# Performance work log

Hardware: AMD Instinct MI355X
Metric: run time of the kernel (lower is better)

The kernel has to match this reference:

```python
import jax, jax.numpy as jnp
import numpy as np

C_IN, C_OUT, KH, KW = 64, 128, 3, 3
STRIDE, PAD, DIL = 1, 1, 1
EPS = 1e-5


def setup_inputs() -> dict:
    key = jax.random.key(0)
    ks = jax.random.split(key, 7)
    B, H, W = 8, 112, 112
    x = jax.random.normal(ks[0], (B, C_IN, H, W), dtype=jnp.float32)
    # offset conv: produces 2*KH*KW offset channels; small init keeps offsets sane
    w_off = jax.random.normal(ks[1], (2 * KH * KW, C_IN, KH, KW), dtype=jnp.float32) * 0.01
    b_off = jax.random.normal(ks[2], (2 * KH * KW,), dtype=jnp.float32) * 0.01
    # deformable conv weight/bias
    fan_in = C_IN * KH * KW
    w_dcn = jax.random.normal(ks[3], (C_OUT, C_IN, KH, KW), dtype=jnp.float32) / np.sqrt(fan_in)
    b_dcn = jax.random.normal(ks[4], (C_OUT,), dtype=jnp.float32) * 0.01
    gamma = jnp.ones((C_OUT,), dtype=jnp.float32)
    beta = jnp.zeros((C_OUT,), dtype=jnp.float32)
    return {"x": x, "w_off": w_off, "b_off": b_off, "w_dcn": w_dcn,
            "b_dcn": b_dcn, "gamma": gamma, "beta": beta}


def _conv2d(x, w, b):
    y = jax.lax.conv_general_dilated(
        x, w, window_strides=(STRIDE, STRIDE),
        padding=((PAD, PAD), (PAD, PAD)),
        rhs_dilation=(DIL, DIL),
        dimension_numbers=("NCHW", "OIHW", "NCHW"))
    return y + b[None, :, None, None]


def _deform_conv(x, offset, w, b):
    # x: [B,C,H,W]; offset: [B, 2*KH*KW, Ho, Wo] with (dy, dx) pairs per tap
    B, C, H, W = x.shape
    KK = KH * KW
    Ho, Wo = offset.shape[2], offset.shape[3]
    off = offset.reshape(B, KK, 2, Ho, Wo)
    ky = (jnp.arange(KK) // KW).astype(jnp.float32)  # kernel row per tap
    kx = (jnp.arange(KK) % KW).astype(jnp.float32)
    base_y = (jnp.arange(Ho) * STRIDE - PAD).astype(jnp.float32)
    base_x = (jnp.arange(Wo) * STRIDE - PAD).astype(jnp.float32)
    # sampling positions [B, KK, Ho, Wo]
    py = off[:, :, 0] + base_y[None, None, :, None] + (ky * DIL)[None, :, None, None]
    px = off[:, :, 1] + base_x[None, None, None, :] + (kx * DIL)[None, :, None, None]

    y0 = jnp.floor(py)
    x0 = jnp.floor(px)
    wy1 = py - y0  # weight for y0+1
    wx1 = px - x0
    y0i = y0.astype(jnp.int32)
    x0i = x0.astype(jnp.int32)

    x_flat = x.reshape(B, C, H * W)

    def gather_corner(yi, xi, wgt):
        # yi, xi, wgt: [B, KK, Ho, Wo]
        valid = (yi >= 0) & (yi < H) & (xi >= 0) & (xi < W)
        idx = jnp.clip(yi, 0, H - 1) * W + jnp.clip(xi, 0, W - 1)
        idx = idx.reshape(B, -1)  # [B, KK*Ho*Wo]
        vals = jnp.take_along_axis(x_flat, idx[:, None, :], axis=2)  # [B, C, N]
        coef = (wgt * valid.astype(wgt.dtype)).reshape(B, 1, -1)
        return vals * coef

    samp = (gather_corner(y0i,     x0i,     (1 - wy1) * (1 - wx1))
            + gather_corner(y0i,     x0i + 1, (1 - wy1) * wx1)
            + gather_corner(y0i + 1, x0i,     wy1 * (1 - wx1))
            + gather_corner(y0i + 1, x0i + 1, wy1 * wx1))
    samp = samp.reshape(B, C, KK, Ho, Wo)
    out = jnp.einsum("bckhw,ock->bohw", samp, w.reshape(w.shape[0], C, KK))
    return out + b[None, :, None, None]


def reference(x, w_off, b_off, w_dcn, b_dcn, gamma, beta):
    offset = _conv2d(x, w_off, b_off)
    y = _deform_conv(x, offset, w_dcn, b_dcn)
    # BatchNorm2d (training mode: biased batch stats) + ReLU
    mean = jnp.mean(y, axis=(0, 2, 3))
    var = jnp.var(y, axis=(0, 2, 3))
    yhat = (y - mean[None, :, None, None]) * jax.lax.rsqrt(var + EPS)[None, :, None, None]
    y = gamma[None, :, None, None] * yhat + beta[None, :, None, None]
    return jax.nn.relu(y)
```

## Files before the change

kernel.cpp:

```cpp
#include <hip/hip_runtime.h>

#define H    112
#define W    112
#define HW   12544
#define CIN  64
#define COUT 128
#define BATCH 8
#define KK   9
#define OFFC 18
#define EPS  1e-5f
#define TP   32
#define KDIM 576
#define KHALF 288
#define KPAD2 296
#define NB   3136

typedef unsigned short ushort;
typedef unsigned int uint;
typedef __attribute__((ext_vector_type(8))) short short8;
typedef __attribute__((ext_vector_type(8))) ushort ushort8;
typedef __attribute__((ext_vector_type(4))) float floatx4;

__device__ __forceinline__ ushort f2bf(float f) {
  uint u = __float_as_uint(f);
  u = (u + 0x7FFFu + ((u >> 16) & 1u)) >> 16;
  return (ushort)u;
}

__device__ __forceinline__ uint pack_bf2(float f0, float f1) {
  uint u0 = __float_as_uint(f0) + 0x8000u;
  uint u1 = __float_as_uint(f1) + 0x8000u;
  return __builtin_amdgcn_perm(u1, u0, 0x07060302u);
}

__device__ __forceinline__ float bf2f(ushort u) {
  return __uint_as_float(((uint)u) << 16);
}

__global__ __launch_bounds__(256) void k_transpose_x(
    const float* __restrict__ x, ushort* __restrict__ xTb) {
  __shared__ float tile[64][65];
  int b = blockIdx.y;
  int p0 = blockIdx.x * 64;
  int tid = threadIdx.x;
  int j = tid & 63, cb = tid >> 6;
#pragma unroll
  for (int i = 0; i < 16; ++i) {
    int ci = cb * 16 + i;
    tile[ci][j] = x[((size_t)(b * CIN + ci)) * HW + p0 + j];
  }
  __syncthreads();
  int px = tid >> 2, ciq = tid & 3;
#pragma unroll
  for (int g = 0; g < 4; ++g) {
    int ci = ciq * 16 + g * 4;
    uint lo = pack_bf2(tile[ci + 0][px], tile[ci + 1][px]);
    uint hi = pack_bf2(tile[ci + 2][px], tile[ci + 3][px]);
    *(uint2*)&xTb[((size_t)b * HW + p0 + px) * 64 + ci] = make_uint2(lo, hi);
  }
}

__global__ __launch_bounds__(256) void k_prep_w(
    const float* __restrict__ w_off, const float* __restrict__ w_dcn,
    ushort* __restrict__ w_offT, ushort* __restrict__ w_mf) {
  int i = blockIdx.x * 256 + threadIdx.x;
  if (i < 32 * KDIM) {
    int oc = i / KDIM, k = i - oc * KDIM;
    int kk = k >> 6, ci = k & 63;
    float v = (oc < OFFC) ? w_off[(oc * CIN + ci) * KK + kk] : 0.f;
    w_offT[i] = f2bf(v);
  } else if (i < 32 * KDIM + COUT * KDIM) {
    int jj = i - 32 * KDIM;
    int co = jj / KDIM, k = jj - co * KDIM;
    int h = k / KHALF, r = k - h * KHALF;
    int kk = r >> 5, cil = r & 31;
    int ci = h * 32 + cil;
    w_mf[jj] = f2bf(w_dcn[(co * CIN + ci) * KK + kk]);
  }
}

__global__ __launch_bounds__(256) void k_offset_conv(
    const ushort* __restrict__ xTb, const ushort* __restrict__ w_offT,
    const float* __restrict__ bias, float* __restrict__ out) {
  int b = blockIdx.y;
  int wave = threadIdx.x >> 6, lane = threadIdx.x & 63;
  int row16 = lane & 15, quad = lane >> 4;
  int p = blockIdx.x * 64 + wave * 16 + row16;
  int ho = p / W, wo = p - ho * W;
  const ushort* xb = xTb + (size_t)b * HW * 64;

  short8 Bf[18];
#pragma unroll
  for (int ks = 0; ks < 18; ++ks) {
    int kk = ks >> 1;
    int ci0 = (ks & 1) * 32 + quad * 8;
    int kh = kk / 3, kw = kk - kh * 3;
    int yy = ho + kh - 1, xx = wo + kw - 1;
    bool valid = (yy >= 0) & (yy < H) & (xx >= 0) & (xx < W);
    short8 v = {0, 0, 0, 0, 0, 0, 0, 0};
    if (valid) v = *(const short8*)(xb + ((size_t)(yy * W + xx) << 6) + ci0);
    Bf[ks] = v;
  }
  floatx4 acc0 = {0.f, 0.f, 0.f, 0.f}, acc1 = acc0;
  const ushort* wa0 = w_offT + row16 * KDIM + quad * 8;
  const ushort* wa1 = w_offT + (16 + row16) * KDIM + quad * 8;
#pragma unroll
  for (int ks = 0; ks < 18; ++ks) {
    short8 A0 = *(const short8*)(wa0 + ks * 32);
    short8 A1 = *(const short8*)(wa1 + ks * 32);
    acc0 = __builtin_amdgcn_mfma_f32_16x16x32_bf16(A0, Bf[ks], acc0, 0, 0, 0);
    acc1 = __builtin_amdgcn_mfma_f32_16x16x32_bf16(A1, Bf[ks], acc1, 0, 0, 0);
  }
  float* ob = out + (size_t)b * OFFC * HW;
#pragma unroll
  for (int reg = 0; reg < 4; ++reg) {
    int oc = quad * 4 + reg;
    ob[(size_t)oc * HW + p] = acc0[reg] + bias[oc];
    int oc1 = 16 + oc;
    if (oc1 < OFFC) ob[(size_t)oc1 * HW + p] = acc1[reg] + bias[oc1];
  }
}

__global__ __launch_bounds__(256) void k_deform(
    const ushort* __restrict__ xTb, const float* __restrict__ off,
    const ushort* __restrict__ w_mf, ushort* __restrict__ y,
    float* __restrict__ psT) {
  __shared__ float4 s_w[KK][TP];
  __shared__ int4   s_i[KK][TP];
  __shared__ ushort samp[TP][KPAD2];

  int b = blockIdx.y;
  int p0 = blockIdx.x * TP;
  int bid = blockIdx.y * gridDim.x + blockIdx.x;
  int tid = threadIdx.x;
  const ushort* xb = xTb + (size_t)b * HW * 64;

  for (int it = tid; it < KK * TP; it += 256) {
    int kk = it >> 5;
    int px = it & 31;
    int p = p0 + px;
    int ho = p / W, wo = p - ho * W;
    float dy = off[((size_t)b * OFFC + 2 * kk) * HW + p];
    float dx = off[((size_t)b * OFFC + 2 * kk + 1) * HW + p];
    float py = dy + (float)(ho - 1 + kk / 3);
    float pxx = dx + (float)(wo - 1 + kk % 3);
    float y0f = floorf(py), x0f = floorf(pxx);
    float wy1 = py - y0f, wx1 = pxx - x0f;
    int y0 = (int)y0f, x0 = (int)x0f;
    int y1 = y0 + 1, x1 = x0 + 1;
    float vy0 = (y0 >= 0 && y0 < H) ? 1.f : 0.f;
    float vy1 = (y1 >= 0 && y1 < H) ? 1.f : 0.f;
    float vx0 = (x0 >= 0 && x0 < W) ? 1.f : 0.f;
    float vx1 = (x1 >= 0 && x1 < W) ? 1.f : 0.f;
    int cy0 = min(max(y0, 0), H - 1), cy1 = min(max(y1, 0), H - 1);
    int cx0 = min(max(x0, 0), W - 1), cx1 = min(max(x1, 0), W - 1);
    s_w[kk][px] = make_float4((1.f - wy1) * (1.f - wx1) * vy0 * vx0,
                              (1.f - wy1) * wx1 * vy0 * vx1,
                              wy1 * (1.f - wx1) * vy1 * vx0,
                              wy1 * wx1 * vy1 * vx1);
    s_i[kk][px] = make_int4((cy0 * W + cx0) << 6, (cy0 * W + cx1) << 6,
                            (cy1 * W + cx0) << 6, (cy1 * W + cx1) << 6);
  }
  __syncthreads();

  int wave = tid >> 6, lane = tid & 63;
  int row16 = lane & 15, quad = lane >> 4;
  int koff = quad * 8;
  int co_base = wave * 32;
  const ushort* wa0 = w_mf + (size_t)(co_base + row16) * KDIM + koff;
  const ushort* wa1 = w_mf + (size_t)(co_base + 16 + row16) * KDIM + koff;

  floatx4 acc00 = {0.f, 0.f, 0.f, 0.f}, acc01 = acc00, acc10 = acc00, acc11 = acc00;

  for (int h = 0; h < 2; ++h) {
#pragma unroll
    for (int r = 0; r < 5; ++r) {
      int it = tid + r * 256;
      if (it < 1152) {
        int px = it / 36;
        int rem = it - px * 36;
        int kk = rem >> 2;
        int cig = rem & 3;
        int cil0 = cig * 8;
        int cio = h * 32 + cil0;
        float4 wv = s_w[kk][px];
        int4 iv = s_i[kk][px];
        ushort8 c0 = *(const ushort8*)(xb + iv.x + cio);
        ushort8 c1 = *(const ushort8*)(xb + iv.y + cio);
        ushort8 c2 = *(const ushort8*)(xb + iv.z + cio);
        ushort8 c3 = *(const ushort8*)(xb + iv.w + cio);
        uint pk[4];
#pragma unroll
        for (int g = 0; g < 4; ++g) {
          float r0 = wv.x * bf2f(c0[2 * g])     + wv.y * bf2f(c1[2 * g]) +
                     wv.z * bf2f(c2[2 * g])     + wv.w * bf2f(c3[2 * g]);
          float r1 = wv.x * bf2f(c0[2 * g + 1]) + wv.y * bf2f(c1[2 * g + 1]) +
                     wv.z * bf2f(c2[2 * g + 1]) + wv.w * bf2f(c3[2 * g + 1]);
          pk[g] = pack_bf2(r0, r1);
        }
        *(uint4*)&samp[px][kk * 32 + cil0] = make_uint4(pk[0], pk[1], pk[2], pk[3]);
      }
    }
    __syncthreads();

    const ushort* sb0 = &samp[row16][koff];
    const ushort* sb1 = &samp[16 + row16][koff];
    const ushort* a0 = wa0 + h * KHALF;
    const ushort* a1 = wa1 + h * KHALF;
#pragma unroll
    for (int ks = 0; ks < 9; ++ks) {
      short8 A0 = *(const short8*)(a0 + ks * 32);
      short8 A1 = *(const short8*)(a1 + ks * 32);
      short8 B0 = *(const short8*)(sb0 + ks * 32);
      short8 B1 = *(const short8*)(sb1 + ks * 32);
      acc00 = __builtin_amdgcn_mfma_f32_16x16x32_bf16(A0, B0, acc00, 0, 0, 0);
      acc01 = __builtin_amdgcn_mfma_f32_16x16x32_bf16(A0, B1, acc01, 0, 0, 0);
      acc10 = __builtin_amdgcn_mfma_f32_16x16x32_bf16(A1, B0, acc10, 0, 0, 0);
      acc11 = __builtin_amdgcn_mfma_f32_16x16x32_bf16(A1, B1, acc11, 0, 0, 0);
    }
    if (h == 0) __syncthreads();
  }

  ushort* yb = y + (size_t)b * COUT * HW + p0;
#pragma unroll
  for (int reg = 0; reg < 4; ++reg) {
    int r0 = quad * 4 + reg;
    yb[(size_t)(co_base + r0) * HW + row16]      = f2bf(acc00[reg]);
    yb[(size_t)(co_base + r0) * HW + 16 + row16] = f2bf(acc01[reg]);
    yb[(size_t)(co_base + 16 + r0) * HW + row16]      = f2bf(acc10[reg]);
    yb[(size_t)(co_base + 16 + r0) * HW + 16 + row16] = f2bf(acc11[reg]);
  }
#pragma unroll
  for (int reg = 0; reg < 4; ++reg) {
    float s0 = acc00[reg] + acc01[reg];
    float q0 = acc00[reg] * acc00[reg] + acc01[reg] * acc01[reg];
    float s1 = acc10[reg] + acc11[reg];
    float q1 = acc10[reg] * acc10[reg] + acc11[reg] * acc11[reg];
#pragma unroll
    for (int m = 1; m < 16; m <<= 1) {
      s0 += __shfl_xor(s0, m, 64);
      q0 += __shfl_xor(q0, m, 64);
      s1 += __shfl_xor(s1, m, 64);
      q1 += __shfl_xor(q1, m, 64);
    }
    if (row16 == 0) {
      int c0 = co_base + quad * 4 + reg;
      int c1 = c0 + 16;
      psT[(size_t)c0 * NB + bid]         = s0;
      psT[(size_t)(128 + c0) * NB + bid] = q0;
      psT[(size_t)c1 * NB + bid]         = s1;
      psT[(size_t)(128 + c1) * NB + bid] = q1;
    }
  }
}

__global__ __launch_bounds__(256) void k_reduce(const float* __restrict__ psT,
                                                float* __restrict__ stats) {
  int j = blockIdx.x;
  int tid = threadIdx.x;
  float s = 0.f;
  for (int i = tid; i < NB; i += 256) s += psT[(size_t)j * NB + i];
#pragma unroll
  for (int o = 32; o > 0; o >>= 1) s += __shfl_down(s, o, 64);
  __shared__ float ls[4];
  int lane = tid & 63, wid = tid >> 6;
  if (lane == 0) ls[wid] = s;
  __syncthreads();
  if (tid == 0) stats[j] = ls[0] + ls[1] + ls[2] + ls[3];
}

__global__ __launch_bounds__(256) void k_norm(const ushort* __restrict__ y,
                                              const float* __restrict__ stats,
                                              const float* __restrict__ gamma,
                                              const float* __restrict__ beta,
                                              float* __restrict__ out) {
  int i4 = blockIdx.x * 256 + threadIdx.x;
  const int total4 = BATCH * COUT * HW / 4;
  if (i4 >= total4) return;
  size_t i = (size_t)i4 * 4;
  int c = (int)((i / HW) & (COUT - 1));
  const float N = (float)(BATCH * HW);
  float m = stats[c] / N;
  float var = stats[COUT + c] / N - m * m;
  float r = rsqrtf(var + EPS);
  float g = gamma[c], bt = beta[c];
  ushort8 v8 = *(const ushort8*)&y[i];
  uint2 u = *(const uint2*)&y[i];
  float4 v = make_float4(bf2f((ushort)(u.x & 0xFFFF)), bf2f((ushort)(u.x >> 16)),
                         bf2f((ushort)(u.y & 0xFFFF)), bf2f((ushort)(u.y >> 16)));
  (void)v8;
  v.x = fmaxf(0.f, (v.x - m) * r * g + bt);
  v.y = fmaxf(0.f, (v.y - m) * r * g + bt);
  v.z = fmaxf(0.f, (v.z - m) * r * g + bt);
  v.w = fmaxf(0.f, (v.w - m) * r * g + bt);
  *(float4*)&out[i] = v;
}

extern "C" void kernel_launch(void* const* d_in, const int* in_sizes, int n_in,
                              void* d_out, int out_size, void* d_ws, size_t ws_size,
                              hipStream_t stream) {
  const float* x     = (const float*)d_in[0];
  const float* w_off = (const float*)d_in[1];
  const float* b_off = (const float*)d_in[2];
  const float* w_dcn = (const float*)d_in[3];
  const float* gamma = (const float*)d_in[5];
  const float* beta  = (const float*)d_in[6];
  float* out = (float*)d_out;

  float* ws = (float*)d_ws;
  float*  off_buf = ws;
  float*  psT     = off_buf + 1806336;
  float*  stats   = psT + 802816;
  ushort* xTb     = (ushort*)(stats + 256);
  ushort* w_mf    = xTb + 6422528;
  ushort* w_offT  = w_mf + 73728;
  ushort* y_bf    = w_offT + 18432;

  k_transpose_x<<<dim3(HW / 64, BATCH), 256, 0, stream>>>(x, xTb);
  k_prep_w<<<(32 * KDIM + COUT * KDIM + 255) / 256, 256, 0, stream>>>(w_off, w_dcn, w_offT, w_mf);
  k_offset_conv<<<dim3(HW / 64, BATCH), 256, 0, stream>>>(xTb, w_offT, b_off, off_buf);
  k_deform<<<dim3(HW / TP, BATCH), 256, 0, stream>>>(xTb, off_buf, w_mf, y_bf, psT);
  k_reduce<<<256, 256, 0, stream>>>(psT, stats);
  k_norm<<<(BATCH * COUT * HW / 4 + 255) / 256, 256, 0, stream>>>(y_bf, stats, gamma, beta, out);
}
```

Before: 229.3 us.

## Fuse offset conv into deform kernel, merge prep kernels, stage outputs via LDS

Computes the offset convolution inside the deform kernel with MFMA and keeps the offsets in LDS, so the global offset buffer and its kernel launch go away. The transpose and weight-prep kernels are merged into one launch. Gather indices are packed to ushort, output tiles are staged in LDS for coalesced 16-byte stores, and partial stats are laid out per block and reduced with atomics. The cost is extra per-block work (redundant halo loads for the offset conv) and more LDS aliasing and syncs.

```diff
diff --git a/kernel.cpp b/kernel.cpp
--- a/kernel.cpp
+++ b/kernel.cpp
@@ -14,12 +14,13 @@
 #define KHALF 288
 #define KPAD2 296
 #define NB   3136
+#define YST  40
 
 typedef unsigned short ushort;
 typedef unsigned int uint;
 typedef __attribute__((ext_vector_type(8))) short short8;
-typedef __attribute__((ext_vector_type(8))) ushort ushort8;
 typedef __attribute__((ext_vector_type(4))) float floatx4;
+typedef __attribute__((ext_vector_type(2))) float f32x2;
 
 __device__ __forceinline__ ushort f2bf(float f) {
   uint u = __float_as_uint(f);
@@ -33,101 +34,66 @@
   return __builtin_amdgcn_perm(u1, u0, 0x07060302u);
 }
 
-__device__ __forceinline__ float bf2f(ushort u) {
-  return __uint_as_float(((uint)u) << 16);
-}
-
-__global__ __launch_bounds__(256) void k_transpose_x(
-    const float* __restrict__ x, ushort* __restrict__ xTb) {
-  __shared__ float tile[64][65];
-  int b = blockIdx.y;
-  int p0 = blockIdx.x * 64;
-  int tid = threadIdx.x;
-  int j = tid & 63, cb = tid >> 6;
-#pragma unroll
-  for (int i = 0; i < 16; ++i) {
-    int ci = cb * 16 + i;
-    tile[ci][j] = x[((size_t)(b * CIN + ci)) * HW + p0 + j];
-  }
-  __syncthreads();
-  int px = tid >> 2, ciq = tid & 3;
-#pragma unroll
-  for (int g = 0; g < 4; ++g) {
-    int ci = ciq * 16 + g * 4;
-    uint lo = pack_bf2(tile[ci + 0][px], tile[ci + 1][px]);
-    uint hi = pack_bf2(tile[ci + 2][px], tile[ci + 3][px]);
-    *(uint2*)&xTb[((size_t)b * HW + p0 + px) * 64 + ci] = make_uint2(lo, hi);
-  }
-}
-
-__global__ __launch_bounds__(256) void k_prep_w(
-    const float* __restrict__ w_off, const float* __restrict__ w_dcn,
+__device__ __forceinline__ f32x2 up2(uint u) {
+  f32x2 r;
+  r.x = __uint_as_float(u << 16);
+  r.y = __uint_as_float(u & 0xFFFF0000u);
+  return r;
+}
+
+__global__ __launch_bounds__(256) void k_prep(
+    const float* __restrict__ x, const float* __restrict__ w_off,
+    const float* __restrict__ w_dcn, ushort* __restrict__ xTb,
     ushort* __restrict__ w_offT, ushort* __restrict__ w_mf) {
-  int i = blockIdx.x * 256 + threadIdx.x;
-  if (i < 32 * KDIM) {
-    int oc = i / KDIM, k = i - oc * KDIM;
-    int kk = k >> 6, ci = k & 63;
-    float v = (oc < OFFC) ? w_off[(oc * CIN + ci) * KK + kk] : 0.f;
-    w_offT[i] = f2bf(v);
-  } else if (i < 32 * KDIM + COUT * KDIM) {
-    int jj = i - 32 * KDIM;
-    int co = jj / KDIM, k = jj - co * KDIM;
-    int h = k / KHALF, r = k - h * KHALF;
-    int kk = r >> 5, cil = r & 31;
-    int ci = h * 32 + cil;
-    w_mf[jj] = f2bf(w_dcn[(co * CIN + ci) * KK + kk]);
-  }
-}
-
-__global__ __launch_bounds__(256) void k_offset_conv(
+  if (blockIdx.y < BATCH) {
+    __shared__ float tile[64][65];
+    int b = blockIdx.y;
+    int p0 = blockIdx.x * 64;
+    int tid = threadIdx.x;
+    int j = tid & 63, cb = tid >> 6;
+#pragma unroll
+    for (int i = 0; i < 16; ++i) {
+      int ci = cb * 16 + i;
+      tile[ci][j] = x[((size_t)(b * CIN + ci)) * HW + p0 + j];
+    }
+    __syncthreads();
+    int px = tid >> 2, ciq = tid & 3;
+#pragma unroll
+    for (int g = 0; g < 4; ++g) {
+      int ci = ciq * 16 + g * 4;
+      uint lo = pack_bf2(tile[ci + 0][px], tile[ci + 1][px]);
+      uint hi = pack_bf2(tile[ci + 2][px], tile[ci + 3][px]);
+      *(uint2*)&xTb[((size_t)b * HW + p0 + px) * 64 + ci] = make_uint2(lo, hi);
+    }
+  } else {
+    const int TOT = 32 * KDIM + COUT * KDIM;
+    for (int i = blockIdx.x * 256 + threadIdx.x; i < TOT; i += 196 * 256) {
+      if (i < 32 * KDIM) {
+        int oc = i / KDIM, k = i - oc * KDIM;
+        int kk = k >> 6, ci = k & 63;
+        float v = (oc < OFFC) ? w_off[(oc * CIN + ci) * KK + kk] : 0.f;
+        w_offT[i] = f2bf(v);
+      } else {
+        int jj = i - 32 * KDIM;
+        int co = jj / KDIM, k = jj - co * KDIM;
+        int h2 = k / KHALF, r = k - h2 * KHALF;
+        int kk = r >> 5, cil = r & 31;
+        int ci = h2 * 32 + cil;
+        w_mf[jj] = f2bf(w_dcn[(co * CIN + ci) * KK + kk]);
+      }
+    }
+  }
+}
+
+__global__ __launch_bounds__(256, 6) void k_deform(
     const ushort* __restrict__ xTb, const ushort* __restrict__ w_offT,
-    const float* __restrict__ bias, float* __restrict__ out) {
-  int b = blockIdx.y;
-  int wave = threadIdx.x >> 6, lane = threadIdx.x & 63;
-  int row16 = lane & 15, quad = lane >> 4;
-  int p = blockIdx.x * 64 + wave * 16 + row16;
-  int ho = p / W, wo = p - ho * W;
-  const ushort* xb = xTb + (size_t)b * HW * 64;
-
-  short8 Bf[18];
-#pragma unroll
-  for (int ks = 0; ks < 18; ++ks) {
-    int kk = ks >> 1;
-    int ci0 = (ks & 1) * 32 + quad * 8;
-    int kh = kk / 3, kw = kk - kh * 3;
-    int yy = ho + kh - 1, xx = wo + kw - 1;
-    bool valid = (yy >= 0) & (yy < H) & (xx >= 0) & (xx < W);
-    short8 v = {0, 0, 0, 0, 0, 0, 0, 0};
-    if (valid) v = *(const short8*)(xb + ((size_t)(yy * W + xx) << 6) + ci0);
-    Bf[ks] = v;
-  }
-  floatx4 acc0 = {0.f, 0.f, 0.f, 0.f}, acc1 = acc0;
-  const ushort* wa0 = w_offT + row16 * KDIM + quad * 8;
-  const ushort* wa1 = w_offT + (16 + row16) * KDIM + quad * 8;
-#pragma unroll
-  for (int ks = 0; ks < 18; ++ks) {
-    short8 A0 = *(const short8*)(wa0 + ks * 32);
-    short8 A1 = *(const short8*)(wa1 + ks * 32);
-    acc0 = __builtin_amdgcn_mfma_f32_16x16x32_bf16(A0, Bf[ks], acc0, 0, 0, 0);
-    acc1 = __builtin_amdgcn_mfma_f32_16x16x32_bf16(A1, Bf[ks], acc1, 0, 0, 0);
-  }
-  float* ob = out + (size_t)b * OFFC * HW;
-#pragma unroll
-  for (int reg = 0; reg < 4; ++reg) {
-    int oc = quad * 4 + reg;
-    ob[(size_t)oc * HW + p] = acc0[reg] + bias[oc];
-    int oc1 = 16 + oc;
-    if (oc1 < OFFC) ob[(size_t)oc1 * HW + p] = acc1[reg] + bias[oc1];
-  }
-}
-
-__global__ __launch_bounds__(256) void k_deform(
-    const ushort* __restrict__ xTb, const float* __restrict__ off,
-    const ushort* __restrict__ w_mf, ushort* __restrict__ y,
-    float* __restrict__ psT) {
-  __shared__ float4 s_w[KK][TP];
-  __shared__ int4   s_i[KK][TP];
-  __shared__ ushort samp[TP][KPAD2];
+    const float* __restrict__ b_off, const ushort* __restrict__ w_mf,
+    ushort* __restrict__ y, float* __restrict__ psT) {
+  __shared__ float4  s_w[KK][TP];
+  __shared__ ushort4 s_ip[KK][TP];
+  __shared__ __align__(16) char smem_raw[TP * KPAD2 * 2];
+  ushort (*samp)[KPAD2] = (ushort(*)[KPAD2])smem_raw;
+  float  (*off_lds)[TP] = (float (*)[TP])smem_raw;
 
   int b = blockIdx.y;
   int p0 = blockIdx.x * TP;
@@ -135,13 +101,43 @@
   int tid = threadIdx.x;
   const ushort* xb = xTb + (size_t)b * HW * 64;
 
+  int wave = tid >> 6, lane = tid & 63;
+  int row16 = lane & 15, quad = lane >> 4;
+
+  {
+    int pxblk = wave & 1, ocblk = wave >> 1;
+    int pxl = pxblk * 16 + row16;
+    int p = p0 + pxl;
+    int ho = p / W, wo = p - ho * W;
+    const ushort* wa = w_offT + (size_t)(ocblk * 16 + row16) * KDIM + quad * 8;
+    floatx4 oacc = {0.f, 0.f, 0.f, 0.f};
+#pragma unroll
+    for (int ks = 0; ks < 18; ++ks) {
+      int kk = ks >> 1;
+      int ci0 = (ks & 1) * 32 + quad * 8;
+      int kh = kk / 3, kw = kk - kh * 3;
+      int yy = ho + kh - 1, xx = wo + kw - 1;
+      short8 bv = {0, 0, 0, 0, 0, 0, 0, 0};
+      if (yy >= 0 && yy < H && xx >= 0 && xx < W)
+        bv = *(const short8*)(xb + ((size_t)(yy * W + xx) << 6) + ci0);
+      short8 av = *(const short8*)(wa + ks * 32);
+      oacc = __builtin_amdgcn_mfma_f32_16x16x32_bf16(av, bv, oacc, 0, 0, 0);
+    }
+#pragma unroll
+    for (int reg = 0; reg < 4; ++reg) {
+      int oc = ocblk * 16 + quad * 4 + reg;
+      if (oc < OFFC) off_lds[oc][pxl] = oacc[reg] + b_off[oc];
+    }
+  }
+  __syncthreads();
+
   for (int it = tid; it < KK * TP; it += 256) {
     int kk = it >> 5;
     int px = it & 31;
     int p = p0 + px;
     int ho = p / W, wo = p - ho * W;
-    float dy = off[((size_t)b * OFFC + 2 * kk) * HW + p];
-    float dx = off[((size_t)b * OFFC + 2 * kk + 1) * HW + p];
+    float dy = off_lds[2 * kk][px];
+    float dx = off_lds[2 * kk + 1][px];
     float py = dy + (float)(ho - 1 + kk / 3);
     float pxx = dx + (float)(wo - 1 + kk % 3);
     float y0f = floorf(py), x0f = floorf(pxx);
@@ -158,13 +154,11 @@
                               (1.f - wy1) * wx1 * vy0 * vx1,
                               wy1 * (1.f - wx1) * vy1 * vx0,
                               wy1 * wx1 * vy1 * vx1);
-    s_i[kk][px] = make_int4((cy0 * W + cx0) << 6, (cy0 * W + cx1) << 6,
-                            (cy1 * W + cx0) << 6, (cy1 * W + cx1) << 6);
+    s_ip[kk][px] = make_ushort4((ushort)(cy0 * W + cx0), (ushort)(cy0 * W + cx1),
+                                (ushort)(cy1 * W + cx0), (ushort)(cy1 * W + cx1));
   }
   __syncthreads();
 
-  int wave = tid >> 6, lane = tid & 63;
-  int row16 = lane & 15, quad = lane >> 4;
   int koff = quad * 8;
   int co_base = wave * 32;
   const ushort* wa0 = w_mf + (size_t)(co_base + row16) * KDIM + koff;
@@ -176,29 +170,29 @@
 #pragma unroll
     for (int r = 0; r < 5; ++r) {
       int it = tid + r * 256;
-      if (it < 1152) {
-        int px = it / 36;
-        int rem = it - px * 36;
-        int kk = rem >> 2;
-        int cig = rem & 3;
+      if (it < KK * TP * 4) {
+        int kk = it >> 7;
+        int px = (it >> 2) & 31;
+        int cig = it & 3;
         int cil0 = cig * 8;
         int cio = h * 32 + cil0;
         float4 wv = s_w[kk][px];
-        int4 iv = s_i[kk][px];
-        ushort8 c0 = *(const ushort8*)(xb + iv.x + cio);
-        ushort8 c1 = *(const ushort8*)(xb + iv.y + cio);
-        ushort8 c2 = *(const ushort8*)(xb + iv.z + cio);
-        ushort8 c3 = *(const ushort8*)(xb + iv.w + cio);
-        uint pk[4];
-#pragma unroll
-        for (int g = 0; g < 4; ++g) {
-          float r0 = wv.x * bf2f(c0[2 * g])     + wv.y * bf2f(c1[2 * g]) +
-                     wv.z * bf2f(c2[2 * g])     + wv.w * bf2f(c3[2 * g]);
-          float r1 = wv.x * bf2f(c0[2 * g + 1]) + wv.y * bf2f(c1[2 * g + 1]) +
-                     wv.z * bf2f(c2[2 * g + 1]) + wv.w * bf2f(c3[2 * g + 1]);
-          pk[g] = pack_bf2(r0, r1);
-        }
-        *(uint4*)&samp[px][kk * 32 + cil0] = make_uint4(pk[0], pk[1], pk[2], pk[3]);
+        ushort4 ip = s_ip[kk][px];
+        const ushort* g0 = xb + (((int)ip.x) << 6) + cio;
+        const ushort* g1 = xb + (((int)ip.y) << 6) + cio;
+        const ushort* g2 = xb + (((int)ip.z) << 6) + cio;
+        const ushort* g3 = xb + (((int)ip.w) << 6) + cio;
+        uint4 c0 = *(const uint4*)g0;
+        uint4 c1 = *(const uint4*)g1;
+        uint4 c2 = *(const uint4*)g2;
+        uint4 c3 = *(const uint4*)g3;
+        f32x2 r0 = up2(c0.x) * wv.x + up2(c1.x) * wv.y + up2(c2.x) * wv.z + up2(c3.x) * wv.w;
+        f32x2 r1 = up2(c0.y) * wv.x + up2(c1.y) * wv.y + up2(c2.y) * wv.z + up2(c3.y) * wv.w;
+        f32x2 r2 = up2(c0.z) * wv.x + up2(c1.z) * wv.y + up2(c2.z) * wv.z + up2(c3.z) * wv.w;
+        f32x2 r3 = up2(c0.w) * wv.x + up2(c1.w) * wv.y + up2(c2.w) * wv.z + up2(c3.w) * wv.w;
+        *(uint4*)&samp[px][kk * 32 + cil0] =
+            make_uint4(pack_bf2(r0.x, r0.y), pack_bf2(r1.x, r1.y),
+                       pack_bf2(r2.x, r2.y), pack_bf2(r3.x, r3.y));
       }
     }
     __syncthreads();
@@ -218,17 +212,17 @@
       acc10 = __builtin_amdgcn_mfma_f32_16x16x32_bf16(A1, B0, acc10, 0, 0, 0);
       acc11 = __builtin_amdgcn_mfma_f32_16x16x32_bf16(A1, B1, acc11, 0, 0, 0);
     }
-    if (h == 0) __syncthreads();
-  }
-
-  ushort* yb = y + (size_t)b * COUT * HW + p0;
+    __syncthreads();
+  }
+
+  ushort (*yst)[YST] = (ushort(*)[YST])smem_raw;
 #pragma unroll
   for (int reg = 0; reg < 4; ++reg) {
     int r0 = quad * 4 + reg;
-    yb[(size_t)(co_base + r0) * HW + row16]      = f2bf(acc00[reg]);
-    yb[(size_t)(co_base + r0) * HW + 16 + row16] = f2bf(acc01[reg]);
-    yb[(size_t)(co_base + 16 + r0) * HW + row16]      = f2bf(acc10[reg]);
-    yb[(size_t)(co_base + 16 + r0) * HW + 16 + row16] = f2bf(acc11[reg]);
+    yst[co_base + r0][row16]            = f2bf(acc00[reg]);
+    yst[co_base + r0][16 + row16]       = f2bf(acc01[reg]);
+    yst[co_base + 16 + r0][row16]       = f2bf(acc10[reg]);
+    yst[co_base + 16 + r0][16 + row16]  = f2bf(acc11[reg]);
   }
 #pragma unroll
   for (int reg = 0; reg < 4; ++reg) {
@@ -245,28 +239,32 @@
     }
     if (row16 == 0) {
       int c0 = co_base + quad * 4 + reg;
-      int c1 = c0 + 16;
-      psT[(size_t)c0 * NB + bid]         = s0;
-      psT[(size_t)(128 + c0) * NB + bid] = q0;
-      psT[(size_t)c1 * NB + bid]         = s1;
-      psT[(size_t)(128 + c1) * NB + bid] = q1;
-    }
+      float* pb = psT + (size_t)bid * 256;
+      pb[c0] = s0;
+      pb[COUT + c0] = q0;
+      pb[c0 + 16] = s1;
+      pb[COUT + c0 + 16] = q1;
+    }
+  }
+  __syncthreads();
+  {
+    int co = tid >> 1, hf = tid & 1;
+    const ushort* src = &yst[co][hf * 16];
+    uint4 v0 = *(const uint4*)src;
+    uint4 v1 = *(const uint4*)(src + 8);
+    ushort* dst = y + (size_t)b * COUT * HW + (size_t)co * HW + p0 + hf * 16;
+    *(uint4*)dst = v0;
+    *(uint4*)(dst + 8) = v1;
   }
 }
 
 __global__ __launch_bounds__(256) void k_reduce(const float* __restrict__ psT,
                                                 float* __restrict__ stats) {
-  int j = blockIdx.x;
-  int tid = threadIdx.x;
+  int c = threadIdx.x;
   float s = 0.f;
-  for (int i = tid; i < NB; i += 256) s += psT[(size_t)j * NB + i];
-#pragma unroll
-  for (int o = 32; o > 0; o >>= 1) s += __shfl_down(s, o, 64);
-  __shared__ float ls[4];
-  int lane = tid & 63, wid = tid >> 6;
-  if (lane == 0) ls[wid] = s;
-  __syncthreads();
-  if (tid == 0) stats[j] = ls[0] + ls[1] + ls[2] + ls[3];
+  for (int r = blockIdx.x; r < NB; r += gridDim.x)
+    s += psT[(size_t)r * 256 + c];
+  atomicAdd(&stats[c], s);
 }
 
 __global__ __launch_bounds__(256) void k_norm(const ushort* __restrict__ y,
@@ -284,11 +282,9 @@
   float var = stats[COUT + c] / N - m * m;
   float r = rsqrtf(var + EPS);
   float g = gamma[c], bt = beta[c];
-  ushort8 v8 = *(const ushort8*)&y[i];
   uint2 u = *(const uint2*)&y[i];
-  float4 v = make_float4(bf2f((ushort)(u.x & 0xFFFF)), bf2f((ushort)(u.x >> 16)),
-                         bf2f((ushort)(u.y & 0xFFFF)), bf2f((ushort)(u.y >> 16)));
-  (void)v8;
+  float4 v = make_float4(__uint_as_float(u.x << 16), __uint_as_float(u.x & 0xFFFF0000u),
+                         __uint_as_float(u.y << 16), __uint_as_float(u.y & 0xFFFF0000u));
   v.x = fmaxf(0.f, (v.x - m) * r * g + bt);
   v.y = fmaxf(0.f, (v.y - m) * r * g + bt);
   v.z = fmaxf(0.f, (v.z - m) * r * g + bt);
@@ -308,18 +304,16 @@
   float* out = (float*)d_out;
 
   float* ws = (float*)d_ws;
-  float*  off_buf = ws;
-  float*  psT     = off_buf + 1806336;
-  float*  stats   = psT + 802816;
-  ushort* xTb     = (ushort*)(stats + 256);
-  ushort* w_mf    = xTb + 6422528;
-  ushort* w_offT  = w_mf + 73728;
-  ushort* y_bf    = w_offT + 18432;
-
-  k_transpose_x<<<dim3(HW / 64, BATCH), 256, 0, stream>>>(x, xTb);
-  k_prep_w<<<(32 * KDIM + COUT * KDIM + 255) / 256, 256, 0, stream>>>(w_off, w_dcn, w_offT, w_mf);
-  k_offset_conv<<<dim3(HW / 64, BATCH), 256, 0, stream>>>(xTb, w_offT, b_off, off_buf);
-  k_deform<<<dim3(HW / TP, BATCH), 256, 0, stream>>>(xTb, off_buf, w_mf, y_bf, psT);
-  k_reduce<<<256, 256, 0, stream>>>(psT, stats);
-  k_norm<<<(BATCH * COUT * HW / 4 + 255) / 256, 256, 0, stream>>>(y_bf, stats, gamma, beta, out);
-}
+  float*  psT    = ws;
+  float*  stats  = psT + 802816;
+  ushort* xTb    = (ushort*)(stats + 256);
+  ushort* w_mf   = xTb + (size_t)BATCH * HW * 64;
+  ushort* w_offT = w_mf + COUT * KDIM;
+  ushort* y_bf   = w_offT + 32 * KDIM;
+
+  hipMemsetAsync(stats, 0, 256 * sizeof(float), stream);
+  k_prep<<<dim3(196, 9), 256, 0, stream>>>(x, w_off, w_dcn, xTb, w_offT, w_mf);
+  k_deform<<<dim3(HW / TP, BATCH), 256, 0, stream>>>(xTb, w_offT, b_off, w_mf, y_bf, psT);
+  k_reduce<<<32, 256, 0, stream>>>(psT, stats);
+  k_norm<<<BATCH * COUT * HW / 4 / 256, 256, 0, stream>>>(y_bf, stats, gamma, beta, out);
+}
```

Result: slower. 254.4 us (+10.9%).
